# Optimization experiments

Hardware: AMD Instinct MI355X
Metric: run time of the kernel (lower is better)

Reference implementation:

```python
import jax, jax.numpy as jnp
import numpy as np

DIM = 1024
HEADS = 16
DIM_HEAD = 64
INNER = HEADS * DIM_HEAD
SCALE = DIM_HEAD ** -0.5
CAUSAL = True


def setup_inputs() -> dict:
    key = jax.random.key(0)
    k1, k2, k3, k4 = jax.random.split(key, 4)
    b, n = 4, 2048
    x = jax.random.normal(k1, (b, n, DIM), dtype=jnp.float32)
    mask = jnp.ones((b, n), dtype=bool)
    w_qkv = jax.random.normal(k2, (DIM, 3 * INNER), dtype=jnp.float32) * (DIM ** -0.5)
    w_out = jax.random.normal(k3, (INNER, DIM), dtype=jnp.float32) * (INNER ** -0.5)
    ln_g = jnp.ones((DIM,), dtype=jnp.float32)
    return {"x": x, "mask": mask, "w_qkv": w_qkv, "w_out": w_out, "ln_g": ln_g}


def clip_layernorm(x, g):
    eps = 1e-5 if x.dtype == jnp.float32 else 1e-3
    mean = jnp.mean(x, axis=-1, keepdims=True)
    var = jnp.var(x, axis=-1, keepdims=True)  # unbiased=False
    return (x - mean) * jax.lax.rsqrt(var + eps) * g


def reference(x, mask, w_qkv, w_out, ln_g):
    b, n, _ = x.shape
    qkv = x @ w_qkv  # [b, n, 3*inner]
    q, k, v = jnp.split(qkv, 3, axis=-1)
    split_heads = lambda t: t.reshape(b, n, HEADS, DIM_HEAD).transpose(0, 2, 1, 3)
    q, k, v = split_heads(q), split_heads(k), split_heads(v)
    q = q * SCALE
    sim = jnp.einsum('bhid,bhjd->bhij', q, k)
    mask_value = -jnp.finfo(sim.dtype).max
    sim = jnp.where(mask[:, None, None, :], sim, mask_value)
    if CAUSAL:
        causal_mask = jnp.triu(jnp.ones((n, n), dtype=bool), k=1)
        sim = jnp.where(causal_mask, mask_value, sim)
    attn = jax.nn.softmax(sim.astype(jnp.float32), axis=-1).astype(sim.dtype)
    out = jnp.einsum('bhij,bhjd->bhid', attn, v)
    out = out.transpose(0, 2, 1, 3).reshape(b, n, INNER)
    out = out @ w_out
    return clip_layernorm(out, ln_g)
```

## Files before the change

### kernel.cpp

```cpp
#include <hip/hip_runtime.h>


typedef unsigned short u16;
typedef __attribute__((ext_vector_type(8))) short bf16x8;
typedef __attribute__((ext_vector_type(4))) float f32x4;
typedef __attribute__((ext_vector_type(4))) unsigned short u16x4;
typedef __attribute__((ext_vector_type(2))) unsigned u32x2;

#define B_SZ  4
#define NSEQ  2048
#define DIMM  1024
#define NQKV  3072
#define MROWS 8192

#define AS_GLOBAL __attribute__((address_space(1)))
#define AS_LDS    __attribute__((address_space(3)))

__device__ __forceinline__ void async_copy16(void* lds, const void* g) {
  __builtin_amdgcn_global_load_lds((const AS_GLOBAL void*)g, (AS_LDS void*)lds, 16, 0, 0);
}

__device__ __forceinline__ u16 f32_to_bf16(float f) {
  unsigned u = __float_as_uint(f);
  u += 0x7FFFu + ((u >> 16) & 1u);
  return (u16)(u >> 16);
}

__device__ __forceinline__ unsigned cvt_pk_bf16(float a, float b) {
  unsigned r;
  asm("v_cvt_pk_bf16_f32 %0, %1, %2" : "=v"(r) : "v"(a), "v"(b));
  return r;
}

template<int N>
__device__ __forceinline__ void wait_lgkm() {
  if constexpr (N == 0)      asm volatile("s_waitcnt lgkmcnt(0)" ::: "memory");
  else if constexpr (N == 2) asm volatile("s_waitcnt lgkmcnt(2)" ::: "memory");
  else if constexpr (N == 4) asm volatile("s_waitcnt lgkmcnt(4)" ::: "memory");
  else if constexpr (N == 6) asm volatile("s_waitcnt lgkmcnt(6)" ::: "memory");
  else if constexpr (N == 8) asm volatile("s_waitcnt lgkmcnt(8)" ::: "memory");
  __builtin_amdgcn_sched_barrier(0);
}


__global__ __launch_bounds__(256) void cvt_bf16_k(const float* __restrict__ in,
                                                  u16* __restrict__ out, int n4) {
  int i = blockIdx.x * 256 + threadIdx.x;
  if (i >= n4) return;
  f32x4 v = ((const f32x4*)in)[i];
  u16x4 o;
  #pragma unroll
  for (int c = 0; c < 4; ++c) o[c] = f32_to_bf16(v[c]);
  ((u16x4*)out)[i] = o;
}

__global__ __launch_bounds__(256) void tconv_k(const float* __restrict__ in,
                                               u16* __restrict__ out, int K, int N) {
  __shared__ float tile[64][65];
  int n0 = blockIdx.x * 64, k0 = blockIdx.y * 64;
  int t = threadIdx.x, tr = t >> 6, tc = t & 63;
  #pragma unroll
  for (int i = 0; i < 16; ++i)
    tile[tr + i * 4][tc] = in[(size_t)(k0 + tr + i * 4) * N + n0 + tc];
  __syncthreads();
  #pragma unroll
  for (int i = 0; i < 16; ++i)
    out[(size_t)(n0 + tr + i * 4) * K + k0 + tc] = f32_to_bf16(tile[tc][tr + i * 4]);
}


template<int BM, int BN, int NW, int MR>
__device__ __forceinline__ void gemm_loop(const u16* __restrict__ A, const u16* __restrict__ Bt,
                                          int K, size_t arow0, size_t brow0,
                                          u16* lA, u16* lB, f32x4 (&acc)[MR][4]) {
  constexpr int WN  = BN / 64;
  constexpr int MH  = MR / 2;
  constexpr int WTM = 16 * MR;
  constexpr int ASZ = BM * 64;
  constexpr int BSZ = BN * 64;
  const int t = threadIdx.x;
  const int w = t >> 6, lane = t & 63;
  const int l4 = lane >> 4, l15 = lane & 15;
  const int wrow = w / WN, wcol = w % WN;
  const int lr = lane >> 3, lc = lane & 7;

  auto stageA = [&](int kt, int bufi, int h) {
    u16* d = lA + bufi * ASZ;
    #pragma unroll
    for (int j = 0; j < BM / (16 * NW); ++j) {
      int r = h * (BM / 2) + w * (BM / (2 * NW)) + j * 8 + lr;
      async_copy16(&d[(size_t)r * 64 + lc * 8],
                   &A[(arow0 + r) * (size_t)K + kt + (lc ^ (r & 7)) * 8]);
    }
  };
  auto stageB = [&](int kt, int bufi, int h) {
    u16* d = lB + bufi * BSZ;
    #pragma unroll
    for (int j = 0; j < BN / (16 * NW); ++j) {
      int r = h * (BN / 2) + w * (BN / (2 * NW)) + j * 8 + lr;
      async_copy16(&d[(size_t)r * 64 + lc * 8],
                   &Bt[(brow0 + r) * (size_t)K + kt + (lc ^ (r & 7)) * 8]);
    }
  };

  auto rdA = [&](const u16* bA, int m, int ch) -> bf16x8 {
    int row = wrow * WTM + m * 16 + l15;
    return *(const bf16x8*)&bA[(size_t)row * 64 + ((ch + l4) ^ (row & 7)) * 8];
  };
  auto rdB = [&](const u16* bB, int n, int ch) -> bf16x8 {
    int row = wcol * 64 + n * 16 + l15;
    return *(const bf16x8*)&bB[(size_t)row * 64 + ((ch + l4) ^ (row & 7)) * 8];
  };

  const int T = K >> 6;
  stageA(0, 0, 0); stageB(0, 0, 0); stageB(0, 0, 1); stageA(0, 0, 1);
  asm volatile("s_waitcnt vmcnt(0)" ::: "memory");
  __builtin_amdgcn_s_barrier();
  __builtin_amdgcn_sched_barrier(0);

  #pragma unroll 1
  for (int s = 0; s < T; ++s) {
    const u16* bA = lA + (s & 1) * ASZ;
    const u16* bB = lB + (s & 1) * BSZ;
    const bool st = (s + 1 < T);
    const int kn = (s + 1) * 64, bn = (s + 1) & 1;
    bf16x8 a0[MH], a1[MH], a2[MH], a3[MH], b0[4], b1[4];

    #pragma unroll
    for (int m = 0; m < MH; ++m) a0[m] = rdA(bA, m, 0);
    #pragma unroll
    for (int n = 0; n < 4; ++n)  b0[n] = rdB(bB, n, 0);
    #pragma unroll
    for (int m = 0; m < MH; ++m) a1[m] = rdA(bA, m, 4);
    #pragma unroll
    for (int n = 0; n < 4; ++n)  b1[n] = rdB(bB, n, 4);
    if (st) { stageA(kn, bn, 0); stageB(kn, bn, 0); }

    wait_lgkm<MH + 4>();
    __builtin_amdgcn_s_setprio(1);
    #pragma unroll
    for (int m = 0; m < MH; ++m)
      #pragma unroll
      for (int n = 0; n < 4; ++n)
        acc[m][n] = __builtin_amdgcn_mfma_f32_16x16x32_bf16(a0[m], b0[n], acc[m][n], 0, 0, 0);
    __builtin_amdgcn_s_setprio(0);

    #pragma unroll
    for (int m = 0; m < MH; ++m) a2[m] = rdA(bA, MH + m, 0);
    if (st) stageB(kn, bn, 1);

    wait_lgkm<MH>();
    __builtin_amdgcn_s_setprio(1);
    #pragma unroll
    for (int m = 0; m < MH; ++m)
      #pragma unroll
      for (int n = 0; n < 4; ++n)
        acc[m][n] = __builtin_amdgcn_mfma_f32_16x16x32_bf16(a1[m], b1[n], acc[m][n], 0, 0, 0);
    __builtin_amdgcn_s_setprio(0);

    #pragma unroll
    for (int m = 0; m < MH; ++m) a3[m] = rdA(bA, MH + m, 4);
    if (st) stageA(kn, bn, 1);

    wait_lgkm<MH>();
    __builtin_amdgcn_s_setprio(1);
    #pragma unroll
    for (int m = 0; m < MH; ++m)
      #pragma unroll
      for (int n = 0; n < 4; ++n)
        acc[MH + m][n] = __builtin_amdgcn_mfma_f32_16x16x32_bf16(a2[m], b0[n], acc[MH + m][n], 0, 0, 0);
    __builtin_amdgcn_s_setprio(0);

    wait_lgkm<0>();
    __builtin_amdgcn_s_setprio(1);
    #pragma unroll
    for (int m = 0; m < MH; ++m)
      #pragma unroll
      for (int n = 0; n < 4; ++n)
        acc[MH + m][n] = __builtin_amdgcn_mfma_f32_16x16x32_bf16(a3[m], b1[n], acc[MH + m][n], 0, 0, 0);
    __builtin_amdgcn_s_setprio(0);

    asm volatile("s_waitcnt vmcnt(0)" ::: "memory");
    __builtin_amdgcn_s_barrier();
    __builtin_amdgcn_sched_barrier(0);
  }
}

__global__ __launch_bounds__(512, 2) void gemm_qkv_k(const u16* __restrict__ A, const u16* __restrict__ Bt,
                                                     u16* __restrict__ qb, u16* __restrict__ kb,
                                                     u16* __restrict__ vtb) {
  __shared__ u16 lA[2 * 256 * 64];
  __shared__ u16 lB[2 * 256 * 64];
  const int id = (int)blockIdx.y * (NQKV / 256) + (int)blockIdx.x;
  const int swz = (id & 7) * 48 + (id >> 3);
  const int bx = swz % (NQKV / 256), by = swz / (NQKV / 256);
  f32x4 acc[8][4];
  #pragma unroll
  for (int m = 0; m < 8; ++m)
    #pragma unroll
    for (int n = 0; n < 4; ++n) acc[m][n] = (f32x4){0.f, 0.f, 0.f, 0.f};
  gemm_loop<256, 256, 8, 8>(A, Bt, DIMM, (size_t)by * 256, (size_t)bx * 256, lA, lB, acc);
  const int t = threadIdx.x, w = t >> 6, lane = t & 63;
  const int l4 = lane >> 4, l15 = lane & 15;
  const int wrow = w >> 2, wcol = w & 3;
  const float QSCALE = 0.125f * 1.44269504089f;
  #pragma unroll
  for (int m = 0; m < 8; ++m)
    #pragma unroll
    for (int n = 0; n < 4; ++n)
      #pragma unroll
      for (int r = 0; r < 4; ++r) {
        int row = by * 256 + wrow * 128 + m * 16 + l4 * 4 + r;
        int col = bx * 256 + wcol * 64 + n * 16 + l15;
        float v = acc[m][n][r];
        int bb = row >> 11, nr = row & 2047;
        int part = col >> 10, rem = col & 1023;
        int h = rem >> 6, d = rem & 63;
        int bh = bb * 16 + h;
        if (part == 0)      qb[((size_t)bh * NSEQ + nr) * 64 + d] = f32_to_bf16(v * QSCALE);
        else if (part == 1) kb[((size_t)bh * NSEQ + nr) * 64 + d] = f32_to_bf16(v);
        else                vtb[((size_t)bh * 64 + d) * NSEQ + nr] = f32_to_bf16(v);
      }
}

__global__ __launch_bounds__(256, 2) void gemm_out_k(const u16* __restrict__ A, const u16* __restrict__ Bt,
                                                     float* __restrict__ C) {
  __shared__ u16 lA[2 * 128 * 64];
  __shared__ u16 lB[2 * 128 * 64];
  const int id = (int)blockIdx.y * (DIMM / 128) + (int)blockIdx.x;
  const int swz = (id & 7) * 64 + (id >> 3);
  const int bx = swz % (DIMM / 128), by = swz / (DIMM / 128);
  f32x4 acc[4][4];
  #pragma unroll
  for (int m = 0; m < 4; ++m)
    #pragma unroll
    for (int n = 0; n < 4; ++n) acc[m][n] = (f32x4){0.f, 0.f, 0.f, 0.f};
  gemm_loop<128, 128, 4, 4>(A, Bt, DIMM, (size_t)by * 128, (size_t)bx * 128, lA, lB, acc);
  const int t = threadIdx.x, w = t >> 6, lane = t & 63;
  const int l4 = lane >> 4, l15 = lane & 15;
  const int wrow = w >> 1, wcol = w & 1;
  #pragma unroll
  for (int m = 0; m < 4; ++m)
    #pragma unroll
    for (int n = 0; n < 4; ++n)
      #pragma unroll
      for (int r = 0; r < 4; ++r) {
        int row = by * 128 + wrow * 64 + m * 16 + l4 * 4 + r;
        int col = bx * 128 + wcol * 64 + n * 16 + l15;
        C[(size_t)row * DIMM + col] = acc[m][n][r];
      }
}


__global__ __launch_bounds__(512, 4) void attn_k(const u16* __restrict__ qb, const u16* __restrict__ kb,
                                                 const u16* __restrict__ vtb, u16* __restrict__ ao) {
  __shared__ u16 lK[2][64 * 64];
  __shared__ u16 lV[2][64 * 64];
  __shared__ u16 lP[8][16 * 64];
  const int bh = blockIdx.y;
  const int t = threadIdx.x, w = t >> 6, l = t & 63;
  const int l4 = l >> 4, l15 = l & 15;
  const int b = bh >> 4, h = bh & 15;
  u16* lPw = lP[w];

  const int srow = t >> 3;
  const int ssc = (t & 7) ^ (srow & 7);

  #pragma unroll 1
  for (int phase = 0; phase < 2; ++phase) {
    const int qt = phase == 0 ? (int)blockIdx.x : 15 - (int)blockIdx.x;
    const int q0w = qt * 128 + w * 16;

    bf16x8 qf0 = *(const bf16x8*)&qb[((size_t)bh * NSEQ + q0w + l15) * 64 + l4 * 8];
    bf16x8 qf1 = *(const bf16x8*)&qb[((size_t)bh * NSEQ + q0w + l15) * 64 + 32 + l4 * 8];

    float m_r = -1e30f, l_r = 0.f;
    f32x4 o[4];
    #pragma unroll
    for (int d = 0; d < 4; ++d) o[d] = (f32x4){0.f, 0.f, 0.f, 0.f};

    const int njt = 2 * qt + 2;

    {
      async_copy16(&lK[0][t * 8], &kb[((size_t)bh * NSEQ + srow) * 64 + ssc * 8]);
      async_copy16(&lV[0][t * 8], &vtb[((size_t)bh * 64 + srow) * NSEQ + ssc * 8]);
    }
    int buf = 0;

    for (int jt = 0; jt < njt; ++jt) {
      __syncthreads();
      if (jt + 1 < njt) {
        int bsel = buf ^ 1, jn = jt + 1;
        async_copy16(&lK[bsel][t * 8], &kb[((size_t)bh * NSEQ + jn * 64 + srow) * 64 + ssc * 8]);
        async_copy16(&lV[bsel][t * 8], &vtb[((size_t)bh * 64 + srow) * NSEQ + (size_t)jn * 64 + ssc * 8]);
      }
      const int jt64 = jt * 64;
      if (jt64 > q0w + 15) { buf ^= 1; continue; }
      const u16* Kb = lK[buf];
      const u16* Vb = lV[buf];

      bf16x8 kf[4][2];
      #pragma unroll
      for (int nf = 0; nf < 4; ++nf)
        #pragma unroll
        for (int kk = 0; kk < 2; ++kk)
          kf[nf][kk] = *(const bf16x8*)&Kb[(nf * 16 + l15) * 64 + ((kk * 4 + l4) ^ (l15 & 7)) * 8];

      f32x4 z[4];
      __builtin_amdgcn_s_setprio(1);
      #pragma unroll
      for (int nf = 0; nf < 4; ++nf) {
        f32x4 zz = (f32x4){0.f, 0.f, 0.f, 0.f};
        zz = __builtin_amdgcn_mfma_f32_16x16x32_bf16(kf[nf][0], qf0, zz, 0, 0, 0);
        zz = __builtin_amdgcn_mfma_f32_16x16x32_bf16(kf[nf][1], qf1, zz, 0, 0, 0);
        z[nf] = zz;
      }
      __builtin_amdgcn_s_setprio(0);

      bf16x8 bv[4][2];
      #pragma unroll
      for (int dd = 0; dd < 4; ++dd)
        #pragma unroll
        for (int kk = 0; kk < 2; ++kk)
          bv[dd][kk] = *(const bf16x8*)&Vb[(dd * 16 + l15) * 64 + ((kk * 4 + l4) ^ (l15 & 7)) * 8];

      if (jt64 + 63 > q0w) {
        #pragma unroll
        for (int nf = 0; nf < 4; ++nf)
          #pragma unroll
          for (int r = 0; r < 4; ++r)
            if (jt64 + nf * 16 + l4 * 4 + r > q0w + l15) z[nf][r] = -1e30f;
      }

      float mt = fmaxf(fmaxf(z[0][0], z[0][1]), fmaxf(z[0][2], z[0][3]));
      #pragma unroll
      for (int nf = 1; nf < 4; ++nf)
        mt = fmaxf(mt, fmaxf(fmaxf(z[nf][0], z[nf][1]), fmaxf(z[nf][2], z[nf][3])));
      mt = fmaxf(mt, __shfl_xor(mt, 16));
      mt = fmaxf(mt, __shfl_xor(mt, 32));

      if (!__all(mt <= m_r + 8.f)) {
        float nm = fmaxf(m_r, mt);
        float sc = __builtin_amdgcn_exp2f(m_r - nm);
        m_r = nm;
        l_r *= sc;
        float scr[4];
        #pragma unroll
        for (int r = 0; r < 4; ++r) scr[r] = __shfl(sc, l4 * 4 + r);
        #pragma unroll
        for (int d = 0; d < 4; ++d)
          #pragma unroll
          for (int r = 0; r < 4; ++r) o[d][r] *= scr[r];
      }

      float rs = 0.f;
      unsigned pk[4][2];
      #pragma unroll
      for (int nf = 0; nf < 4; ++nf)
        #pragma unroll
        for (int hh = 0; hh < 2; ++hh) {
          float p0 = __builtin_amdgcn_exp2f(z[nf][2 * hh]     - m_r);
          float p1 = __builtin_amdgcn_exp2f(z[nf][2 * hh + 1] - m_r);
          rs += p0 + p1;
          pk[nf][hh] = cvt_pk_bf16(p0, p1);
        }
      rs += __shfl_xor(rs, 16);
      rs += __shfl_xor(rs, 32);
      l_r += rs;

      #pragma unroll
      for (int nf = 0; nf < 4; ++nf) {
        int u = (2 * nf + (l4 >> 1)) ^ (l15 & 7);
        *(u32x2*)&lPw[l15 * 64 + u * 8 + (l4 & 1) * 4] = (u32x2){pk[nf][0], pk[nf][1]};
      }
      __builtin_amdgcn_sched_barrier(0);
      int u0 = l4 ^ (l15 & 7), u1 = (4 + l4) ^ (l15 & 7);
      bf16x8 af0 = *(const bf16x8*)&lPw[l15 * 64 + u0 * 8];
      bf16x8 af1 = *(const bf16x8*)&lPw[l15 * 64 + u1 * 8];

      __builtin_amdgcn_s_setprio(1);
      #pragma unroll
      for (int d = 0; d < 4; ++d) {
        o[d] = __builtin_amdgcn_mfma_f32_16x16x32_bf16(af0, bv[d][0], o[d], 0, 0, 0);
        o[d] = __builtin_amdgcn_mfma_f32_16x16x32_bf16(af1, bv[d][1], o[d], 0, 0, 0);
      }
      __builtin_amdgcn_s_setprio(0);
      buf ^= 1;
    }

    float lv[4];
    #pragma unroll
    for (int r = 0; r < 4; ++r) lv[r] = __shfl(l_r, l4 * 4 + r);
    #pragma unroll
    for (int d = 0; d < 4; ++d)
      #pragma unroll
      for (int r = 0; r < 4; ++r) {
        int nrow = q0w + l4 * 4 + r;
        float vv = o[d][r] / lv[r];
        ao[((size_t)(b * NSEQ + nrow)) * 1024 + h * 64 + d * 16 + l15] = f32_to_bf16(vv);
      }
  }
}

__global__ __launch_bounds__(256) void ln_k(float* __restrict__ io, const float* __restrict__ g) {
  const int row = blockIdx.x, t = threadIdx.x;
  const int w = t >> 6, l = t & 63;
  f32x4 v = ((const f32x4*)(io + (size_t)row * DIMM))[t];
  float s = v[0] + v[1] + v[2] + v[3];
  float q = v[0] * v[0] + v[1] * v[1] + v[2] * v[2] + v[3] * v[3];
  #pragma unroll
  for (int off = 1; off < 64; off <<= 1) { s += __shfl_xor(s, off); q += __shfl_xor(q, off); }
  __shared__ float ss[8];
  if (l == 0) { ss[w] = s; ss[4 + w] = q; }
  __syncthreads();
  s = ss[0] + ss[1] + ss[2] + ss[3];
  q = ss[4] + ss[5] + ss[6] + ss[7];
  float mean = s * (1.f / DIMM);
  float var = q * (1.f / DIMM) - mean * mean;
  float rstd = rsqrtf(var + 1e-5f);
  f32x4 gv = ((const f32x4*)g)[t];
  f32x4 y;
  #pragma unroll
  for (int c = 0; c < 4; ++c) y[c] = (v[c] - mean) * rstd * gv[c];
  ((f32x4*)(io + (size_t)row * DIMM))[t] = y;
}

extern "C" void kernel_launch(void* const* d_in, const int* in_sizes, int n_in,
                              void* d_out, int out_size, void* d_ws, size_t ws_size,
                              hipStream_t stream) {
  const float* x     = (const float*)d_in[0];
  const float* w_qkv = (const float*)d_in[2];
  const float* w_out = (const float*)d_in[3];
  const float* ln_g  = (const float*)d_in[4];
  float* out = (float*)d_out;

  char* ws = (char*)d_ws;
  const size_t MB = 1u << 20;
  u16* x_bf   = (u16*)(ws);
  u16* wqkv_t = (u16*)(ws + 16 * MB);
  u16* wout_t = (u16*)(ws + 22 * MB);
  u16* qb     = (u16*)(ws + 24 * MB);
  u16* kb     = (u16*)(ws + 40 * MB);
  u16* vtb    = (u16*)(ws + 56 * MB);
  u16* attn_o = x_bf;

  cvt_bf16_k<<<8192, 256, 0, stream>>>(x, x_bf, (MROWS * DIMM) / 4);
  tconv_k<<<dim3(NQKV / 64, DIMM / 64), 256, 0, stream>>>(w_qkv, wqkv_t, DIMM, NQKV);
  tconv_k<<<dim3(DIMM / 64, DIMM / 64), 256, 0, stream>>>(w_out, wout_t, DIMM, DIMM);
  gemm_qkv_k<<<dim3(NQKV / 256, MROWS / 256), 512, 0, stream>>>(x_bf, wqkv_t, qb, kb, vtb);
  attn_k<<<dim3(8, B_SZ * 16), 512, 0, stream>>>(qb, kb, vtb, attn_o);
  gemm_out_k<<<dim3(DIMM / 128, MROWS / 128), 256, 0, stream>>>(attn_o, wout_t, out);
  ln_k<<<MROWS, 256, 0, stream>>>(out, ln_g);
}
```

Before: 205.3 us.

## Restructure GEMM pipeline into K-half stages and widen output GEMM tile

The shared GEMM loop now splits each 64-wide K tile into two 32-wide halves, each with its own LDS layout and XOR swizzle. Global-to-LDS copies for the next tile are issued per half and waited on with partial vmcnt counts, replacing the full vmcnt(0) drain at the end of every iteration, so loads overlap MFMA work more. The output projection GEMM moves to 128x256 tiles with 512 threads. The aim is to hide memory latency and cut barrier stalls, at the cost of more barriers per iteration and more LDS per output-GEMM block.

```diff
diff --git a/kernel.cpp b/kernel.cpp
--- a/kernel.cpp
+++ b/kernel.cpp
@@ -32,13 +32,15 @@
   return r;
 }
 
-template<int N>
-__device__ __forceinline__ void wait_lgkm() {
-  if constexpr (N == 0)      asm volatile("s_waitcnt lgkmcnt(0)" ::: "memory");
-  else if constexpr (N == 2) asm volatile("s_waitcnt lgkmcnt(2)" ::: "memory");
-  else if constexpr (N == 4) asm volatile("s_waitcnt lgkmcnt(4)" ::: "memory");
-  else if constexpr (N == 6) asm volatile("s_waitcnt lgkmcnt(6)" ::: "memory");
-  else if constexpr (N == 8) asm volatile("s_waitcnt lgkmcnt(8)" ::: "memory");
+__device__ __forceinline__ void wait_lgkm0() {
+  asm volatile("s_waitcnt lgkmcnt(0)" ::: "memory");
+  __builtin_amdgcn_sched_barrier(0);
+}
+template<int N> __device__ __forceinline__ void wait_vm() {
+  if constexpr (N == 0)      asm volatile("s_waitcnt vmcnt(0)" ::: "memory");
+  else if constexpr (N == 3) asm volatile("s_waitcnt vmcnt(3)" ::: "memory");
+  else if constexpr (N == 4) asm volatile("s_waitcnt vmcnt(4)" ::: "memory");
+  else if constexpr (N == 6) asm volatile("s_waitcnt vmcnt(6)" ::: "memory");
   __builtin_amdgcn_sched_barrier(0);
 }
 
@@ -73,116 +75,122 @@
 __device__ __forceinline__ void gemm_loop(const u16* __restrict__ A, const u16* __restrict__ Bt,
                                           int K, size_t arow0, size_t brow0,
                                           u16* lA, u16* lB, f32x4 (&acc)[MR][4]) {
-  constexpr int WN  = BN / 64;
-  constexpr int MH  = MR / 2;
-  constexpr int WTM = 16 * MR;
-  constexpr int ASZ = BM * 64;
-  constexpr int BSZ = BN * 64;
+  constexpr int NT   = NW * 64;
+  constexpr int WN   = BN / 64;
+  constexpr int MH   = MR / 2;
+  constexpr int WTM  = 16 * MR;
+  constexpr int ABUF = BM * 64;
+  constexpr int BBUF = BN * 64;
+  constexpr int AHALF = BM * 32;
+  constexpr int BHALF = BN * 32;
+  constexpr int AI = (4 * BM) / NT;
+  constexpr int BI = (4 * BN) / NT;
+  constexpr int VN = AI + BI;
   const int t = threadIdx.x;
   const int w = t >> 6, lane = t & 63;
   const int l4 = lane >> 4, l15 = lane & 15;
   const int wrow = w / WN, wcol = w % WN;
-  const int lr = lane >> 3, lc = lane & 7;
-
-  auto stageA = [&](int kt, int bufi, int h) {
-    u16* d = lA + bufi * ASZ;
-    #pragma unroll
-    for (int j = 0; j < BM / (16 * NW); ++j) {
-      int r = h * (BM / 2) + w * (BM / (2 * NW)) + j * 8 + lr;
-      async_copy16(&d[(size_t)r * 64 + lc * 8],
-                   &A[(arow0 + r) * (size_t)K + kt + (lc ^ (r & 7)) * 8]);
+
+  auto stageA = [&](int kt, int kh, int bufi) {
+    u16* d = lA + bufi * ABUF + kh * AHALF;
+    #pragma unroll
+    for (int j = 0; j < AI; ++j) {
+      int c = j * NT + t;
+      int row = c >> 2, q = c & 3;
+      int sq = q ^ ((row >> 1) & 3);
+      async_copy16(&d[(size_t)c * 8],
+                   &A[(arow0 + row) * (size_t)K + kt + kh * 32 + sq * 8]);
     }
   };
-  auto stageB = [&](int kt, int bufi, int h) {
-    u16* d = lB + bufi * BSZ;
-    #pragma unroll
-    for (int j = 0; j < BN / (16 * NW); ++j) {
-      int r = h * (BN / 2) + w * (BN / (2 * NW)) + j * 8 + lr;
-      async_copy16(&d[(size_t)r * 64 + lc * 8],
-                   &Bt[(brow0 + r) * (size_t)K + kt + (lc ^ (r & 7)) * 8]);
+  auto stageB = [&](int kt, int kh, int bufi) {
+    u16* d = lB + bufi * BBUF + kh * BHALF;
+    #pragma unroll
+    for (int j = 0; j < BI; ++j) {
+      int c = j * NT + t;
+      int row = c >> 2, q = c & 3;
+      int sq = q ^ ((row >> 1) & 3);
+      async_copy16(&d[(size_t)c * 8],
+                   &Bt[(brow0 + row) * (size_t)K + kt + kh * 32 + sq * 8]);
     }
   };
 
-  auto rdA = [&](const u16* bA, int m, int ch) -> bf16x8 {
+  auto rdA = [&](int bufi, int kk, int m) -> bf16x8 {
     int row = wrow * WTM + m * 16 + l15;
-    return *(const bf16x8*)&bA[(size_t)row * 64 + ((ch + l4) ^ (row & 7)) * 8];
+    return *(const bf16x8*)&lA[bufi * ABUF + kk * AHALF + (size_t)row * 32 +
+                               ((l4 ^ ((row >> 1) & 3))) * 8];
   };
-  auto rdB = [&](const u16* bB, int n, int ch) -> bf16x8 {
+  auto rdB = [&](int bufi, int kk, int n) -> bf16x8 {
     int row = wcol * 64 + n * 16 + l15;
-    return *(const bf16x8*)&bB[(size_t)row * 64 + ((ch + l4) ^ (row & 7)) * 8];
+    return *(const bf16x8*)&lB[bufi * BBUF + kk * BHALF + (size_t)row * 32 +
+                               ((l4 ^ ((row >> 1) & 3))) * 8];
   };
 
   const int T = K >> 6;
-  stageA(0, 0, 0); stageB(0, 0, 0); stageB(0, 0, 1); stageA(0, 0, 1);
-  asm volatile("s_waitcnt vmcnt(0)" ::: "memory");
-  __builtin_amdgcn_s_barrier();
-  __builtin_amdgcn_sched_barrier(0);
+  stageA(0, 0, 0); stageB(0, 0, 0); stageA(0, 1, 0); stageB(0, 1, 0);
 
   #pragma unroll 1
   for (int s = 0; s < T; ++s) {
-    const u16* bA = lA + (s & 1) * ASZ;
-    const u16* bB = lB + (s & 1) * BSZ;
+    const int bufR = s & 1, bufW = bufR ^ 1;
     const bool st = (s + 1 < T);
-    const int kn = (s + 1) * 64, bn = (s + 1) & 1;
-    bf16x8 a0[MH], a1[MH], a2[MH], a3[MH], b0[4], b1[4];
-
-    #pragma unroll
-    for (int m = 0; m < MH; ++m) a0[m] = rdA(bA, m, 0);
-    #pragma unroll
-    for (int n = 0; n < 4; ++n)  b0[n] = rdB(bB, n, 0);
-    #pragma unroll
-    for (int m = 0; m < MH; ++m) a1[m] = rdA(bA, m, 4);
-    #pragma unroll
-    for (int n = 0; n < 4; ++n)  b1[n] = rdB(bB, n, 4);
-    if (st) { stageA(kn, bn, 0); stageB(kn, bn, 0); }
-
-    wait_lgkm<MH + 4>();
-    __builtin_amdgcn_s_setprio(1);
-    #pragma unroll
-    for (int m = 0; m < MH; ++m)
-      #pragma unroll
-      for (int n = 0; n < 4; ++n)
-        acc[m][n] = __builtin_amdgcn_mfma_f32_16x16x32_bf16(a0[m], b0[n], acc[m][n], 0, 0, 0);
-    __builtin_amdgcn_s_setprio(0);
-
-    #pragma unroll
-    for (int m = 0; m < MH; ++m) a2[m] = rdA(bA, MH + m, 0);
-    if (st) stageB(kn, bn, 1);
-
-    wait_lgkm<MH>();
-    __builtin_amdgcn_s_setprio(1);
-    #pragma unroll
-    for (int m = 0; m < MH; ++m)
-      #pragma unroll
-      for (int n = 0; n < 4; ++n)
-        acc[m][n] = __builtin_amdgcn_mfma_f32_16x16x32_bf16(a1[m], b1[n], acc[m][n], 0, 0, 0);
-    __builtin_amdgcn_s_setprio(0);
-
-    #pragma unroll
-    for (int m = 0; m < MH; ++m) a3[m] = rdA(bA, MH + m, 4);
-    if (st) stageA(kn, bn, 1);
-
-    wait_lgkm<MH>();
-    __builtin_amdgcn_s_setprio(1);
-    #pragma unroll
-    for (int m = 0; m < MH; ++m)
-      #pragma unroll
-      for (int n = 0; n < 4; ++n)
-        acc[MH + m][n] = __builtin_amdgcn_mfma_f32_16x16x32_bf16(a2[m], b0[n], acc[MH + m][n], 0, 0, 0);
-    __builtin_amdgcn_s_setprio(0);
-
-    wait_lgkm<0>();
-    __builtin_amdgcn_s_setprio(1);
-    #pragma unroll
-    for (int m = 0; m < MH; ++m)
-      #pragma unroll
-      for (int n = 0; n < 4; ++n)
-        acc[MH + m][n] = __builtin_amdgcn_mfma_f32_16x16x32_bf16(a3[m], b1[n], acc[MH + m][n], 0, 0, 0);
-    __builtin_amdgcn_s_setprio(0);
-
-    asm volatile("s_waitcnt vmcnt(0)" ::: "memory");
+    const int kn = (s + 1) * 64;
+    bf16x8 af[MH], bf[4];
+
+    wait_vm<VN>();
     __builtin_amdgcn_s_barrier();
     __builtin_amdgcn_sched_barrier(0);
+    #pragma unroll
+    for (int m = 0; m < MH; ++m) af[m] = rdA(bufR, 0, m);
+    #pragma unroll
+    for (int n = 0; n < 4; ++n)  bf[n] = rdB(bufR, 0, n);
+    if (st) stageA(kn, 0, bufW);
+    wait_lgkm0();
+    __builtin_amdgcn_s_setprio(1);
+    #pragma unroll
+    for (int m = 0; m < MH; ++m)
+      #pragma unroll
+      for (int n = 0; n < 4; ++n)
+        acc[m][n] = __builtin_amdgcn_mfma_f32_16x16x32_bf16(af[m], bf[n], acc[m][n], 0, 0, 0);
+    __builtin_amdgcn_s_setprio(0);
+    #pragma unroll
+    for (int m = 0; m < MH; ++m) af[m] = rdA(bufR, 0, MH + m);
+    if (st) stageB(kn, 0, bufW);
+    wait_lgkm0();
+    __builtin_amdgcn_s_setprio(1);
+    #pragma unroll
+    for (int m = 0; m < MH; ++m)
+      #pragma unroll
+      for (int n = 0; n < 4; ++n)
+        acc[MH + m][n] = __builtin_amdgcn_mfma_f32_16x16x32_bf16(af[m], bf[n], acc[MH + m][n], 0, 0, 0);
+    __builtin_amdgcn_s_setprio(0);
+
+    if (st) wait_vm<VN>();
+    else    wait_vm<0>();
+    __builtin_amdgcn_s_barrier();
+    __builtin_amdgcn_sched_barrier(0);
+    #pragma unroll
+    for (int m = 0; m < MH; ++m) af[m] = rdA(bufR, 1, m);
+    #pragma unroll
+    for (int n = 0; n < 4; ++n)  bf[n] = rdB(bufR, 1, n);
+    if (st) stageA(kn, 1, bufW);
+    wait_lgkm0();
+    __builtin_amdgcn_s_setprio(1);
+    #pragma unroll
+    for (int m = 0; m < MH; ++m)
+      #pragma unroll
+      for (int n = 0; n < 4; ++n)
+        acc[m][n] = __builtin_amdgcn_mfma_f32_16x16x32_bf16(af[m], bf[n], acc[m][n], 0, 0, 0);
+    __builtin_amdgcn_s_setprio(0);
+    #pragma unroll
+    for (int m = 0; m < MH; ++m) af[m] = rdA(bufR, 1, MH + m);
+    if (st) stageB(kn, 1, bufW);
+    wait_lgkm0();
+    __builtin_amdgcn_s_setprio(1);
+    #pragma unroll
+    for (int m = 0; m < MH; ++m)
+      #pragma unroll
+      for (int n = 0; n < 4; ++n)
+        acc[MH + m][n] = __builtin_amdgcn_mfma_f32_16x16x32_bf16(af[m], bf[n], acc[MH + m][n], 0, 0, 0);
+    __builtin_amdgcn_s_setprio(0);
   }
 }
 
@@ -223,22 +231,22 @@
       }
 }
 
-__global__ __launch_bounds__(256, 2) void gemm_out_k(const u16* __restrict__ A, const u16* __restrict__ Bt,
+__global__ __launch_bounds__(512, 2) void gemm_out_k(const u16* __restrict__ A, const u16* __restrict__ Bt,
                                                      float* __restrict__ C) {
   __shared__ u16 lA[2 * 128 * 64];
-  __shared__ u16 lB[2 * 128 * 64];
-  const int id = (int)blockIdx.y * (DIMM / 128) + (int)blockIdx.x;
-  const int swz = (id & 7) * 64 + (id >> 3);
-  const int bx = swz % (DIMM / 128), by = swz / (DIMM / 128);
+  __shared__ u16 lB[2 * 256 * 64];
+  const int id = (int)blockIdx.y * (DIMM / 256) + (int)blockIdx.x;
+  const int swz = (id & 7) * 32 + (id >> 3);
+  const int bx = swz % (DIMM / 256), by = swz / (DIMM / 256);
   f32x4 acc[4][4];
   #pragma unroll
   for (int m = 0; m < 4; ++m)
     #pragma unroll
     for (int n = 0; n < 4; ++n) acc[m][n] = (f32x4){0.f, 0.f, 0.f, 0.f};
-  gemm_loop<128, 128, 4, 4>(A, Bt, DIMM, (size_t)by * 128, (size_t)bx * 128, lA, lB, acc);
+  gemm_loop<128, 256, 8, 4>(A, Bt, DIMM, (size_t)by * 128, (size_t)bx * 256, lA, lB, acc);
   const int t = threadIdx.x, w = t >> 6, lane = t & 63;
   const int l4 = lane >> 4, l15 = lane & 15;
-  const int wrow = w >> 1, wcol = w & 1;
+  const int wrow = w >> 2, wcol = w & 3;
   #pragma unroll
   for (int m = 0; m < 4; ++m)
     #pragma unroll
@@ -246,7 +254,7 @@
       #pragma unroll
       for (int r = 0; r < 4; ++r) {
         int row = by * 128 + wrow * 64 + m * 16 + l4 * 4 + r;
-        int col = bx * 128 + wcol * 64 + n * 16 + l15;
+        int col = bx * 256 + wcol * 64 + n * 16 + l15;
         C[(size_t)row * DIMM + col] = acc[m][n][r];
       }
 }
@@ -449,6 +457,6 @@
   tconv_k<<<dim3(DIMM / 64, DIMM / 64), 256, 0, stream>>>(w_out, wout_t, DIMM, DIMM);
   gemm_qkv_k<<<dim3(NQKV / 256, MROWS / 256), 512, 0, stream>>>(x_bf, wqkv_t, qb, kb, vtb);
   attn_k<<<dim3(8, B_SZ * 16), 512, 0, stream>>>(qb, kb, vtb, attn_o);
-  gemm_out_k<<<dim3(DIMM / 128, MROWS / 128), 256, 0, stream>>>(attn_o, wout_t, out);
+  gemm_out_k<<<dim3(DIMM / 256, MROWS / 128), 512, 0, stream>>>(attn_o, wout_t, out);
   ln_k<<<MROWS, 256, 0, stream>>>(out, ln_g);
 }
```

Result: no change. 207.2 us (+0.9%).
